# Kernel optimization log

Measured on AMD Instinct MI355X. Metric: run time of the kernel, lower is better.

Reference implementation:

```python
import jax, jax.numpy as jnp
import numpy as np

B, L, D, H, M = 4, 2048, 256, 8, 256
HEAD = D // H
EPS = 1e-6


def _pos_embedding(maxlen, d):
    i = np.arange(maxlen, dtype=np.float64)[:, None]
    j = np.arange(d, dtype=np.float64)[None, :]
    angle = i / np.power(10000.0, (j - (j % 2)) / d)
    pe = np.where(j % 2 == 0, np.sin(angle), np.cos(angle))
    return jnp.asarray(pe, jnp.float32)  # [L, D]


def _projection_matrix(m, d, seed=0):
    # FAVOR+ orthogonal random features: one full QR block (m == d here),
    # rows rescaled by norms of iid Gaussian rows (scaling=0 in source).
    rng = np.random.default_rng(seed)
    block = rng.standard_normal((d, d))
    q, _ = np.linalg.qr(block)
    q = q.T[:m]
    mult = np.linalg.norm(rng.standard_normal((m, d)), axis=1)
    return jnp.asarray(mult[:, None] * q, jnp.float32)  # [M, D]


def _softmax_kernel(x, is_query, proj):
    # x: [B, L, H, D], proj: [M, D]
    d = x.shape[-1]
    m = proj.shape[0]
    x = x * (float(d) ** -0.25)
    xp = jnp.einsum('blhd,md->blhm', x, proj)
    diag = 0.5 * jnp.sum(x * x, axis=-1, keepdims=True)
    if is_query:
        mx = jnp.max(xp, axis=-1, keepdims=True)
    else:
        mx = jnp.max(xp, axis=(-3, -1), keepdims=True)  # over L and M
    return (float(m) ** -0.5) * (jnp.exp(xp - diag - mx) + EPS)


def setup_inputs() -> dict:
    key = jax.random.key(0)
    ks = jax.random.split(key, 12)
    s = 1.0 / np.sqrt(D)
    inp = {
        'query': jax.random.normal(ks[0], (B, L, D), jnp.float32),
        'key': jax.random.normal(ks[1], (B, L, D), jnp.float32),
        'value': jax.random.normal(ks[2], (B, L, D), jnp.float32),
        'mask': jnp.ones((B, L), jnp.float32),
        'Wq': jax.random.normal(ks[3], (D, D), jnp.float32) * s,
        'bq': jnp.zeros((D,), jnp.float32),
        'Wk': jax.random.normal(ks[4], (D, D), jnp.float32) * s,
        'bk': jnp.zeros((D,), jnp.float32),
        'Wv': jax.random.normal(ks[5], (D, D), jnp.float32) * s,
        'bv': jnp.zeros((D,), jnp.float32),
        'Wo': jax.random.normal(ks[6], (D, D), jnp.float32) * s,
        'bo': jnp.zeros((D,), jnp.float32),
        'proj': _projection_matrix(M, D, seed=0),
        'pos': _pos_embedding(L, D),
    }
    return inp


def reference(query, key, value, mask, Wq, bq, Wk, bk, Wv, bv, Wo, bo, proj, pos):
    b = query.shape[0]
    q = query @ Wq + bq                      # [B, L, D]
    k = key @ Wk + bk
    v = value @ Wv + bv
    # per-head copies keep the FULL model_size feature dim (as in source)
    q = jnp.broadcast_to(q[:, :, None, :], (b, L, H, D))
    k = jnp.broadcast_to(k[:, :, None, :], (b, L, H, D))
    pos_b = pos[None]                        # [1, L, D]
    cos_pos = jnp.repeat(pos_b[..., None, 1::2], 2, axis=-1)  # [1, L, 1, D]
    sin_pos = jnp.repeat(pos_b[..., None, ::2], 2, axis=-1)

    def rot(x):
        x2 = jnp.stack([-x[..., 1::2], x[..., ::2]], axis=-1).reshape(x.shape)
        return x * cos_pos + x2 * sin_pos

    q = rot(q)
    k = rot(k)
    v = v.reshape(b, L, H, HEAD)

    qp = _softmax_kernel(q, True, proj)      # [B, L, H, M]
    kp = _softmax_kernel(k, False, proj)     # [B, L, H, M]

    kvs = jnp.einsum('blhm,blhd->bhmd', kp, v)
    num = jnp.einsum('blhm,bhmd->blhd', qp, kvs)
    den = jnp.einsum('blhm,bhm->blh', qp, jnp.sum(kp, axis=1))
    ctx = (num / den[..., None]).reshape(b, L, D)
    return ctx @ Wo + bo
```

## Files before the change

### kernel.cpp

```cpp
#include <hip/hip_runtime.h>

typedef unsigned short u16;
typedef unsigned int u32;
typedef __bf16 bf16x8 __attribute__((ext_vector_type(8)));
typedef float f32x4 __attribute__((ext_vector_type(4)));

__device__ __forceinline__ float bf2f(u16 u) { return __uint_as_float(((u32)u) << 16); }
__device__ __forceinline__ u16 f2bf(float f) {
  u32 x = __float_as_uint(f);
  x += 0x7fffu + ((x >> 16) & 1u);
  return (u16)(x >> 16);
}
__device__ __forceinline__ u32 encf(float x) {
  u32 u = __float_as_uint(x);
  return (u >> 31) ? ~u : (u | 0x80000000u);
}
__device__ __forceinline__ float decf(u32 e) {
  return (e >> 31) ? __uint_as_float(e & 0x7fffffffu) : __uint_as_float(~e);
}

#define MFMA(a, b, c) __builtin_amdgcn_mfma_f32_16x16x32_bf16(a, b, c, 0, 0, 0)

__global__ __launch_bounds__(256) void prep_w(
    const float* Wq, const float* Wk, const float* Wv, const float* Wo,
    const float* proj, const float* bv,
    u16* WqT, u16* WkT, u16* projb, u16* WWT, float* bw,
    float* __restrict__ ksum, u32* __restrict__ mxk) {
  __shared__ u16 tsh[32][33];
  __shared__ u16 As[64][40];
  __shared__ u16 Bs[64][40];
  const int z = blockIdx.z;
  const int x = threadIdx.x, y = threadIdx.y;
  const int tid = y * 32 + x;
  if (z < 2) {
    const float* s = z == 0 ? Wq : Wk;
    u16* d = z == 0 ? WqT : WkT;
    int r0 = blockIdx.y * 32, c0 = blockIdx.x * 32;
#pragma unroll
    for (int i = 0; i < 32; i += 8) tsh[y + i][x] = f2bf(s[(r0 + y + i) * 256 + c0 + x]);
    __syncthreads();
#pragma unroll
    for (int i = 0; i < 32; i += 8) d[(c0 + y + i) * 256 + r0 + x] = tsh[x][y + i];
    return;
  }
  if (z == 2) {
    int r0 = blockIdx.y * 32, c0 = blockIdx.x * 32;
#pragma unroll
    for (int i = 0; i < 32; i += 8)
      projb[(r0 + y + i) * 256 + c0 + x] = f2bf(proj[(r0 + y + i) * 256 + c0 + x]);
    return;
  }
  if (blockIdx.x < 4 && blockIdx.y < 4) {
    const int o0 = blockIdx.x * 64, i0 = blockIdx.y * 64;
    const int lane = tid & 63, wid = tid >> 6;
    const int wm = (wid >> 1) * 32, wn = (wid & 1) * 32;
    const int fm = lane & 15, fq = (lane >> 4) * 8, rowq = (lane >> 4) * 4;
    const int dr = tid >> 3, oc = (tid & 7) * 8;
    const int ir = tid >> 2, dc = (tid & 3) * 8;
    f32x4 acc[2][2] = {};
    for (int it = 0; it < 8; ++it) {
      int d0 = it * 32;
      float4 w0 = *(const float4*)(Wo + (d0 + dr) * 256 + o0 + oc);
      float4 w1 = *(const float4*)(Wo + (d0 + dr) * 256 + o0 + oc + 4);
      float4 v0 = *(const float4*)(Wv + (i0 + ir) * 256 + d0 + dc);
      float4 v1 = *(const float4*)(Wv + (i0 + ir) * 256 + d0 + dc + 4);
      __syncthreads();
      float wv[8] = {w0.x, w0.y, w0.z, w0.w, w1.x, w1.y, w1.z, w1.w};
#pragma unroll
      for (int j = 0; j < 8; ++j) As[oc + j][dr] = f2bf(wv[j]);
      u16* bp = &Bs[ir][dc];
      bp[0] = f2bf(v0.x); bp[1] = f2bf(v0.y); bp[2] = f2bf(v0.z); bp[3] = f2bf(v0.w);
      bp[4] = f2bf(v1.x); bp[5] = f2bf(v1.y); bp[6] = f2bf(v1.z); bp[7] = f2bf(v1.w);
      __syncthreads();
      bf16x8 a0 = *(const bf16x8*)&As[wm + fm][fq];
      bf16x8 a1 = *(const bf16x8*)&As[wm + 16 + fm][fq];
      bf16x8 b0 = *(const bf16x8*)&Bs[wn + fm][fq];
      bf16x8 b1 = *(const bf16x8*)&Bs[wn + 16 + fm][fq];
      acc[0][0] = MFMA(a0, b0, acc[0][0]);
      acc[0][1] = MFMA(a0, b1, acc[0][1]);
      acc[1][0] = MFMA(a1, b0, acc[1][0]);
      acc[1][1] = MFMA(a1, b1, acc[1][1]);
    }
#pragma unroll
    for (int mt = 0; mt < 2; ++mt)
#pragma unroll
      for (int nt = 0; nt < 2; ++nt)
#pragma unroll
        for (int r = 0; r < 4; ++r)
          WWT[(o0 + wm + mt * 16 + rowq + r) * 256 + i0 + wn + nt * 16 + fm] =
              f2bf(acc[mt][nt][r]);
    return;
  }
  if (blockIdx.x == 4 && blockIdx.y == 0) {
    float s = 0.0f;
    for (int d = 0; d < 256; ++d) s = fmaf(bv[d], Wo[d * 256 + tid], s);
    bw[tid] = s;
    for (int i = tid; i < 1024; i += 256) ksum[i] = 0.0f;
    if (tid < 4) mxk[tid] = 0u;
  }
}

__global__ __launch_bounds__(256, 3) void projrot2(
    const float* __restrict__ Xq, const float* __restrict__ Xk,
    const u16* __restrict__ WqT, const u16* __restrict__ WkT,
    const float* __restrict__ bq, const float* __restrict__ bk,
    const float* __restrict__ pos, const u16* __restrict__ projb,
    float* __restrict__ diag_k, u16* __restrict__ qp,
    float* __restrict__ xp, u32* __restrict__ mxk) {
  const int mode = blockIdx.z;
  const float* X = mode ? Xq : Xk;
  const u16* W = mode ? WqT : WkT;
  const float* bias = mode ? bq : bk;
  __shared__ u16 As[32][40];
  __shared__ u16 Bs[256][40];
  __shared__ u16 cbuf[32][264];
  __shared__ float dred[2][32];
  __shared__ float mred[2][32];
  __shared__ float wred[4];
  const int row0 = blockIdx.x * 32;
  const int t = threadIdx.x;
  const int lane = t & 63, wid = t >> 6;
  const int wrow = wid & 1, wcol = wid >> 1;
  const int fm = lane & 15, fq = (lane >> 4) * 8, rowq = (lane >> 4) * 4;
  const int ar = t >> 3, ak = (t & 7) * 4;

  f32x4 acc[8] = {};
  float4 av = *(const float4*)(X + (long long)(row0 + ar) * 256 + ak);
  uint4 bv0 = ((const uint4*)(W + (long long)t * 256))[0];
  uint4 bv1 = ((const uint4*)(W + (long long)t * 256))[1];
  uint4 bv2 = ((const uint4*)(W + (long long)t * 256))[2];
  uint4 bv3 = ((const uint4*)(W + (long long)t * 256))[3];
  for (int s = 0; s < 8; ++s) {
    __syncthreads();
    As[ar][ak] = f2bf(av.x); As[ar][ak + 1] = f2bf(av.y);
    As[ar][ak + 2] = f2bf(av.z); As[ar][ak + 3] = f2bf(av.w);
    uint4* bsp = (uint4*)&Bs[t][0];
    bsp[0] = bv0; bsp[1] = bv1; bsp[2] = bv2; bsp[3] = bv3;
    __syncthreads();
    if (s < 7) {
      const int k1 = (s + 1) * 32;
      av = *(const float4*)(X + (long long)(row0 + ar) * 256 + k1 + ak);
      const uint4* wn = (const uint4*)(W + (long long)t * 256 + k1);
      bv0 = wn[0]; bv1 = wn[1]; bv2 = wn[2]; bv3 = wn[3];
    }
    bf16x8 af = *(const bf16x8*)&As[wrow * 16 + fm][fq];
#pragma unroll
    for (int j = 0; j < 8; ++j) {
      bf16x8 bf = *(const bf16x8*)&Bs[wcol * 128 + j * 16 + fm][fq];
      acc[j] = MFMA(af, bf, acc[j]);
    }
  }

  float dsum[4] = {};
#pragma unroll
  for (int j = 0; j < 8; ++j) {
    float bb2 = bias[wcol * 128 + j * 16 + fm];
#pragma unroll
    for (int r = 0; r < 4; ++r) {
      float v = acc[j][r] + bb2;
      acc[j][r] = v;
      dsum[r] += v * v;
    }
  }
#pragma unroll
  for (int o = 1; o < 16; o <<= 1)
#pragma unroll
    for (int r = 0; r < 4; ++r) dsum[r] += __shfl_xor(dsum[r], o, 64);
  if (fm == 0) {
#pragma unroll
    for (int r = 0; r < 4; ++r) dred[wcol][wrow * 16 + rowq + r] = dsum[r];
  }
  __syncthreads();
  if (mode == 0 && t < 32) diag_k[row0 + t] = 0.03125f * (dred[0][t] + dred[1][t]);

#pragma unroll
  for (int j = 0; j < 8; ++j) {
    const int c = wcol * 128 + j * 16 + fm;
#pragma unroll
    for (int r = 0; r < 4; ++r) {
      const int row = wrow * 16 + rowq + r;
      const int l = (row0 + row) & 2047;
      float v = acc[j][r];
      float prt = __shfl_xor(v, 1, 64);
      float x2 = (fm & 1) ? prt : -prt;
      float2 cs = *(const float2*)(pos + (long long)l * 256 + (c & ~1));
      cbuf[row][c] = f2bf(0.25f * (v * cs.y + x2 * cs.x));
    }
  }

  f32x4 acc2[8] = {};
  uint4 pv0 = ((const uint4*)(projb + (long long)t * 256))[0];
  uint4 pv1 = ((const uint4*)(projb + (long long)t * 256))[1];
  uint4 pv2 = ((const uint4*)(projb + (long long)t * 256))[2];
  uint4 pv3 = ((const uint4*)(projb + (long long)t * 256))[3];
  for (int s = 0; s < 8; ++s) {
    __syncthreads();
    uint4* bsp = (uint4*)&Bs[t][0];
    bsp[0] = pv0; bsp[1] = pv1; bsp[2] = pv2; bsp[3] = pv3;
    __syncthreads();
    if (s < 7) {
      const uint4* pn = (const uint4*)(projb + (long long)t * 256 + (s + 1) * 32);
      pv0 = pn[0]; pv1 = pn[1]; pv2 = pn[2]; pv3 = pn[3];
    }
    bf16x8 af = *(const bf16x8*)&cbuf[wrow * 16 + fm][s * 32 + fq];
#pragma unroll
    for (int j = 0; j < 8; ++j) {
      bf16x8 bf = *(const bf16x8*)&Bs[wcol * 128 + j * 16 + fm][fq];
      acc2[j] = MFMA(af, bf, acc2[j]);
    }
  }

  if (mode == 1) {
    float m4[4] = {-3.0e38f, -3.0e38f, -3.0e38f, -3.0e38f};
#pragma unroll
    for (int j = 0; j < 8; ++j)
#pragma unroll
      for (int r = 0; r < 4; ++r) m4[r] = fmaxf(m4[r], acc2[j][r]);
#pragma unroll
    for (int o = 1; o < 16; o <<= 1)
#pragma unroll
      for (int r = 0; r < 4; ++r) m4[r] = fmaxf(m4[r], __shfl_xor(m4[r], o, 64));
    if (fm == 0) {
#pragma unroll
      for (int r = 0; r < 4; ++r) mred[wcol][wrow * 16 + rowq + r] = m4[r];
    }
    __syncthreads();
#pragma unroll
    for (int j = 0; j < 8; ++j) {
      const int col = wcol * 128 + j * 16 + fm;
#pragma unroll
      for (int r = 0; r < 4; ++r) {
        const int row = wrow * 16 + rowq + r;
        float mxr = fmaxf(mred[0][row], mred[1][row]);
        float dgr = 0.03125f * (dred[0][row] + dred[1][row]);
        float v = 0.0625f * (__expf(acc2[j][r] - dgr - mxr) + 1e-6f);
        qp[(long long)(row0 + row) * 256 + col] = f2bf(v);
      }
    }
  } else {
    float mx = -3.0e38f;
#pragma unroll
    for (int j = 0; j < 8; ++j) {
      int col = wcol * 128 + j * 16 + fm;
#pragma unroll
      for (int r = 0; r < 4; ++r) {
        float v = acc2[j][r];
        xp[(long long)(row0 + wrow * 16 + rowq + r) * 256 + col] = v;
        mx = fmaxf(mx, v);
      }
    }
#pragma unroll
    for (int o = 32; o > 0; o >>= 1) mx = fmaxf(mx, __shfl_xor(mx, o, 64));
    if (lane == 0) wred[wid] = mx;
    __syncthreads();
    if (t == 0) {
      float m = fmaxf(fmaxf(wred[0], wred[1]), fmaxf(wred[2], wred[3]));
      atomicMax(mxk + (row0 >> 11), encf(m));
    }
  }
}

__global__ __launch_bounds__(256) void kvs_raw_split(
    const float* __restrict__ xp, const float* __restrict__ Xv,
    const float* __restrict__ diag_k, const u32* __restrict__ mxk,
    float* __restrict__ part, float* __restrict__ ksum) {
  __shared__ union USM {
    struct { u16 As[64][40]; u16 Bs[64][40]; } s;
    float ksbuf[32][65];
  } sm;
  const int mxt = blockIdx.x, ny = blockIdx.y, z = blockIdx.z;
  const int b = z >> 2, kc = z & 3;
  const long long l0 = (long long)b * 2048 + kc * 512;
  const int t = threadIdx.x;
  const int lane = t & 63, wid = t >> 6;
  const int wrow = wid >> 1, wcol = wid & 1;
  const int fm = lane & 15, fq = (lane >> 4) * 8, rowq = (lane >> 4) * 4;
  const float mxv = decf(mxk[b]);
  const int sr = t >> 3, sc = (t & 7) * 8;
  f32x4 acc[2][2] = {};
  float ksp[8] = {};
  long long lrow = l0 + sr;
  float4 x0 = *(const float4*)(xp + lrow * 256 + mxt * 64 + sc);
  float4 x1 = *(const float4*)(xp + lrow * 256 + mxt * 64 + sc + 4);
  float4 v0 = *(const float4*)(Xv + lrow * 256 + ny * 64 + sc);
  float4 v1 = *(const float4*)(Xv + lrow * 256 + ny * 64 + sc + 4);
  float dgl = diag_k[lrow];
  for (int s = 0; s < 16; ++s) {
    float xv[8] = {x0.x, x0.y, x0.z, x0.w, x1.x, x1.y, x1.z, x1.w};
    float vv[8] = {v0.x, v0.y, v0.z, v0.w, v1.x, v1.y, v1.z, v1.w};
    u16 kpv[8], vpv[8];
#pragma unroll
    for (int j = 0; j < 8; ++j) {
      float v = 0.0625f * (__expf(xv[j] - dgl - mxv) + 1e-6f);
      kpv[j] = f2bf(v);
      ksp[j] += bf2f(kpv[j]);
      vpv[j] = f2bf(vv[j]);
    }
    __syncthreads();
#pragma unroll
    for (int j = 0; j < 8; ++j) {
      sm.s.As[sc + j][sr] = kpv[j];
      sm.s.Bs[sc + j][sr] = vpv[j];
    }
    __syncthreads();
    if (s < 15) {
      lrow = l0 + (s + 1) * 32 + sr;
      x0 = *(const float4*)(xp + lrow * 256 + mxt * 64 + sc);
      x1 = *(const float4*)(xp + lrow * 256 + mxt * 64 + sc + 4);
      v0 = *(const float4*)(Xv + lrow * 256 + ny * 64 + sc);
      v1 = *(const float4*)(Xv + lrow * 256 + ny * 64 + sc + 4);
      dgl = diag_k[lrow];
    }
    bf16x8 a0 = *(const bf16x8*)&sm.s.As[wrow * 32 + fm][fq];
    bf16x8 a1 = *(const bf16x8*)&sm.s.As[wrow * 32 + 16 + fm][fq];
    bf16x8 b0 = *(const bf16x8*)&sm.s.Bs[wcol * 32 + fm][fq];
    bf16x8 b1 = *(const bf16x8*)&sm.s.Bs[wcol * 32 + 16 + fm][fq];
    acc[0][0] = MFMA(a0, b0, acc[0][0]);
    acc[0][1] = MFMA(a0, b1, acc[0][1]);
    acc[1][0] = MFMA(a1, b0, acc[1][0]);
    acc[1][1] = MFMA(a1, b1, acc[1][1]);
  }
#pragma unroll
  for (int mt = 0; mt < 2; ++mt)
#pragma unroll
    for (int nt = 0; nt < 2; ++nt)
#pragma unroll
      for (int r = 0; r < 4; ++r)
        part[(long long)z * 65536 +
             (long long)(mxt * 64 + wrow * 32 + mt * 16 + rowq + r) * 256 +
             ny * 64 + wcol * 32 + nt * 16 + fm] = acc[mt][nt][r];
  __syncthreads();
#pragma unroll
  for (int j = 0; j < 8; ++j) sm.ksbuf[sr][sc + j] = ksp[j];
  __syncthreads();
  if (ny == 0 && t < 64) {
    float ssum = 0.0f;
    for (int r = 0; r < 32; ++r) ssum += sm.ksbuf[r][t];
    atomicAdd(ksum + b * 256 + mxt * 64 + t, ssum);
  }
}

__global__ __launch_bounds__(256) void kvsw(
    const u16* __restrict__ WWT, const float* __restrict__ part,
    const float* __restrict__ ksum, const float* __restrict__ bw,
    u16* __restrict__ kvsWT) {
  __shared__ u16 As[64][40];
  __shared__ u16 Bs[64][40];
  const int o0 = blockIdx.x * 64, m0 = blockIdx.y * 64, b = blockIdx.z;
  const int t = threadIdx.x;
  const int lane = t & 63, wid = t >> 6;
  const int wm = (wid >> 1) * 32, wn = (wid & 1) * 32;
  const int fm = lane & 15, fq = (lane >> 4) * 8, rowq = (lane >> 4) * 4;
  const int arow = t >> 2, acol = (t & 3) * 8;
  f32x4 acc[2][2] = {};
  for (int it = 0; it < 8; ++it) {
    int k0 = it * 32;
    uint4 av = *(const uint4*)(WWT + (o0 + arow) * 256 + k0 + acol);
    float4 s0 = {0, 0, 0, 0}, s1 = {0, 0, 0, 0};
#pragma unroll
    for (int kc = 0; kc < 4; ++kc) {
      const float* pp = part + (long long)(b * 4 + kc) * 65536 + (long long)(m0 + arow) * 256 + k0 + acol;
      float4 u0 = *(const float4*)(pp);
      float4 u1 = *(const float4*)(pp + 4);
      s0.x += u0.x; s0.y += u0.y; s0.z += u0.z; s0.w += u0.w;
      s1.x += u1.x; s1.y += u1.y; s1.z += u1.z; s1.w += u1.w;
    }
    __syncthreads();
    *(uint4*)&As[arow][acol] = av;
    u16* bp = &Bs[arow][acol];
    bp[0] = f2bf(s0.x); bp[1] = f2bf(s0.y); bp[2] = f2bf(s0.z); bp[3] = f2bf(s0.w);
    bp[4] = f2bf(s1.x); bp[5] = f2bf(s1.y); bp[6] = f2bf(s1.z); bp[7] = f2bf(s1.w);
    __syncthreads();
    bf16x8 a0 = *(const bf16x8*)&As[wm + fm][fq];
    bf16x8 a1 = *(const bf16x8*)&As[wm + 16 + fm][fq];
    bf16x8 b0 = *(const bf16x8*)&Bs[wn + fm][fq];
    bf16x8 b1 = *(const bf16x8*)&Bs[wn + 16 + fm][fq];
    acc[0][0] = MFMA(a0, b0, acc[0][0]);
    acc[0][1] = MFMA(a0, b1, acc[0][1]);
    acc[1][0] = MFMA(a1, b0, acc[1][0]);
    acc[1][1] = MFMA(a1, b1, acc[1][1]);
  }
#pragma unroll
  for (int mt = 0; mt < 2; ++mt)
#pragma unroll
    for (int nt = 0; nt < 2; ++nt) {
      int col = m0 + wn + nt * 16 + fm;
      float ksv = ksum[b * 256 + col];
#pragma unroll
      for (int r = 0; r < 4; ++r) {
        int row = o0 + wm + mt * 16 + rowq + r;
        float v = acc[mt][nt][r] + bw[row] * ksv;
        kvsWT[(long long)b * 65536 + (long long)row * 256 + col] = f2bf(v);
      }
    }
}

__global__ __launch_bounds__(256, 4) void numout(
    const u16* __restrict__ qp, const float* __restrict__ ksum,
    const u16* __restrict__ kvsWT, const float* __restrict__ bo,
    float* __restrict__ out) {
  __shared__ u16 As[16][40];
  __shared__ u16 Bs[256][40];
  __shared__ float ksm[256], dsh[16];
  const int row0 = blockIdx.x * 16;
  const int b = blockIdx.z;
  const long long qrow = (long long)b * 2048 + row0;
  const int t = threadIdx.x;
  const int lane = t & 63, wid = t >> 6;
  const int fm = lane & 15, fq = (lane >> 4) * 8, rowq = (lane >> 4) * 4;
  const int ar = t >> 4, ak = (t & 15) * 2;

  u32 a0 = *(const u32*)(qp + (qrow + ar) * 256 + ak);
  const u16* kvr = kvsWT + (long long)b * 65536 + (long long)t * 256;
  uint4 bv0 = ((const uint4*)kvr)[0];
  uint4 bv1 = ((const uint4*)kvr)[1];
  uint4 bv2 = ((const uint4*)kvr)[2];
  uint4 bv3 = ((const uint4*)kvr)[3];

  ksm[t] = ksum[b * 256 + t];
  const int prow = t >> 4, pc0 = (t & 15) * 16;
  const u16* qr = qp + (qrow + prow) * 256 + pc0;
  uint4 u0 = *(const uint4*)(qr);
  uint4 u1 = *(const uint4*)(qr + 8);
  __syncthreads();

  float denp = 0.0f;
  u32 uu[8] = {u0.x, u0.y, u0.z, u0.w, u1.x, u1.y, u1.z, u1.w};
#pragma unroll
  for (int j = 0; j < 8; ++j) {
    denp += bf2f((u16)(uu[j] & 0xffffu)) * ksm[pc0 + 2 * j];
    denp += bf2f((u16)(uu[j] >> 16)) * ksm[pc0 + 2 * j + 1];
  }
#pragma unroll
  for (int o = 1; o < 16; o <<= 1) denp += __shfl_xor(denp, o, 64);
  if ((t & 15) == 0) dsh[prow] = denp;

  f32x4 acc[4] = {};
  for (int s = 0; s < 8; ++s) {
    __syncthreads();
    *(u32*)&As[ar][ak] = a0;
    uint4* bsp = (uint4*)&Bs[t][0];
    bsp[0] = bv0; bsp[1] = bv1; bsp[2] = bv2; bsp[3] = bv3;
    __syncthreads();
    if (s < 7) {
      const int k1 = (s + 1) * 32;
      a0 = *(const u32*)(qp + (qrow + ar) * 256 + k1 + ak);
      const uint4* kn = (const uint4*)(kvr + k1);
      bv0 = kn[0]; bv1 = kn[1]; bv2 = kn[2]; bv3 = kn[3];
    }
    bf16x8 af = *(const bf16x8*)&As[fm][fq];
#pragma unroll
    for (int j = 0; j < 4; ++j) {
      bf16x8 bf = *(const bf16x8*)&Bs[wid * 64 + j * 16 + fm][fq];
      acc[j] = MFMA(af, bf, acc[j]);
    }
  }
#pragma unroll
  for (int j = 0; j < 4; ++j) {
    int col = wid * 64 + j * 16 + fm;
    float bb2 = bo[col];
#pragma unroll
    for (int r = 0; r < 4; ++r) {
      int l = rowq + r;
      out[(qrow + l) * 256 + col] = acc[j][r] / dsh[l] + bb2;
    }
  }
}

extern "C" void kernel_launch(void* const* d_in, const int* in_sizes, int n_in,
                              void* d_out, int out_size, void* d_ws, size_t ws_size,
                              hipStream_t stream) {
  (void)in_sizes; (void)n_in; (void)out_size; (void)ws_size;
  const float* query = (const float*)d_in[0];
  const float* key = (const float*)d_in[1];
  const float* value = (const float*)d_in[2];
  const float* Wq = (const float*)d_in[4];
  const float* bq = (const float*)d_in[5];
  const float* Wk = (const float*)d_in[6];
  const float* bk = (const float*)d_in[7];
  const float* Wv = (const float*)d_in[8];
  const float* bv = (const float*)d_in[9];
  const float* Wo = (const float*)d_in[10];
  const float* bo = (const float*)d_in[11];
  const float* proj = (const float*)d_in[12];
  const float* pos = (const float*)d_in[13];

  char* w = (char*)d_ws;
  u16* qp = (u16*)(w);
  float* xp = (float*)(w + (8 << 20));
  float* part = (float*)(w + (16 << 20));
  u16* kvsWT = (u16*)(w + (20 << 20));
  u16* WqT = (u16*)(w + (21 << 20));
  u16* WkT = WqT + 65536;
  u16* projb = WkT + 65536;
  u16* WWT = projb + 65536;
  float* diag_k = (float*)(w + (22 << 20));
  float* ksum = diag_k + 8192;
  float* bw = ksum + 1024;
  u32* mxk = (u32*)(bw + 256);

  prep_w<<<dim3(8, 8, 4), dim3(32, 8), 0, stream>>>(Wq, Wk, Wv, Wo, proj, bv,
                                                    WqT, WkT, projb, WWT, bw,
                                                    ksum, mxk);
  projrot2<<<dim3(256, 1, 2), dim3(256), 0, stream>>>(
      query, key, WqT, WkT, bq, bk, pos, projb, diag_k, qp, xp, mxk);
  kvs_raw_split<<<dim3(4, 4, 16), dim3(256), 0, stream>>>(xp, value, diag_k, mxk,
                                                          part, ksum);
  kvsw<<<dim3(4, 4, 4), dim3(256), 0, stream>>>(WWT, part, ksum, bw, kvsWT);
  numout<<<dim3(128, 1, 4), dim3(256), 0, stream>>>(qp, ksum, kvsWT, bo,
                                                    (float*)d_out);
}
```

Baseline: 81.12 us.

## Fuse all stages into one persistent kernel with grid-wide atomic barriers

Replaces the five separate kernel launches with a single 512-block persistent kernel. The stages (weight prep, Q/K projection with rotary and feature map, KV partial sums, KV times W reduction, output) are separated by software grid barriers built on an atomic counter. The k-split of the KV reduction also changes from 4 to 8 chunks per batch. This removes per-launch overhead and the inter-kernel gaps, but it relies on all 512 blocks being co-resident (launch bounds of 2 blocks per CU) and adds a memset plus spin-wait cost at each barrier.

New measurement: 250.9 us. +209.3%, slower.

```diff
diff --git a/kernel.cpp b/kernel.cpp
--- a/kernel.cpp
+++ b/kernel.cpp
@@ -21,61 +21,311 @@
 
 #define MFMA(a, b, c) __builtin_amdgcn_mfma_f32_16x16x32_bf16(a, b, c, 0, 0, 0)
 
-__global__ __launch_bounds__(256) void prep_w(
-    const float* Wq, const float* Wk, const float* Wv, const float* Wo,
-    const float* proj, const float* bv,
-    u16* WqT, u16* WkT, u16* projb, u16* WWT, float* bw,
-    float* __restrict__ ksum, u32* __restrict__ mxk) {
-  __shared__ u16 tsh[32][33];
-  __shared__ u16 As[64][40];
-  __shared__ u16 Bs[64][40];
-  const int z = blockIdx.z;
-  const int x = threadIdx.x, y = threadIdx.y;
-  const int tid = y * 32 + x;
-  if (z < 2) {
-    const float* s = z == 0 ? Wq : Wk;
-    u16* d = z == 0 ? WqT : WkT;
-    int r0 = blockIdx.y * 32, c0 = blockIdx.x * 32;
-#pragma unroll
-    for (int i = 0; i < 32; i += 8) tsh[y + i][x] = f2bf(s[(r0 + y + i) * 256 + c0 + x]);
+__device__ __forceinline__ void gbar(u32* cnt, u32 target) {
+  __syncthreads();
+  if (threadIdx.x == 0) {
+    __hip_atomic_fetch_add(cnt, 1u, __ATOMIC_RELEASE, __HIP_MEMORY_SCOPE_AGENT);
+    while (__hip_atomic_load(cnt, __ATOMIC_RELAXED, __HIP_MEMORY_SCOPE_AGENT) < target)
+      __builtin_amdgcn_s_sleep(2);
+    __threadfence();
+  }
+  __syncthreads();
+}
+
+struct MegaArgs {
+  const float* Xq; const float* Xk; const float* Xv;
+  const float* Wq; const float* bq; const float* Wk; const float* bk;
+  const float* Wv; const float* bv; const float* Wo; const float* bo;
+  const float* proj; const float* pos;
+  u16* WqT; u16* WkT; u16* projb; u16* WWT; u16* qp; u16* kvsWT;
+  float* xp; float* part; float* diag_k; float* ksum; float* bw;
+  u32* mxk; float* out; u32* bar;
+};
+
+union SMU {
+  struct { u16 tsh[32][33]; } t;
+  struct { u16 As[64][40]; u16 Bs[64][40]; } g;
+  struct { float ksbuf[32][65]; } k;
+  struct { u16 As[32][40]; u16 Bs[256][40]; u16 cbuf[32][264];
+           float dred[2][32]; float mred[2][32]; float wred[4]; } b;
+  struct { u16 As[64][40]; u16 Bs[16][40]; } d;
+  struct { u16 As[16][40]; u16 Bs[256][40];
+           float ksm[256]; float dsh[16]; } e;
+};
+
+__global__ __launch_bounds__(256, 2) void mega(MegaArgs a) {
+  __shared__ SMU sm;
+  const int bid = blockIdx.x;
+  const int t = threadIdx.x;
+
+  {
+    const int x = t & 31, y = t >> 5;
+    if (bid < 192) {
+      const int which = bid >> 6;
+      const int sub = bid & 63;
+      const int c0 = (sub & 7) * 32, r0 = (sub >> 3) * 32;
+      if (which < 2) {
+        const float* s = which == 0 ? a.Wq : a.Wk;
+        u16* d = which == 0 ? a.WqT : a.WkT;
+#pragma unroll
+        for (int i = 0; i < 32; i += 8)
+          sm.t.tsh[y + i][x] = f2bf(s[(r0 + y + i) * 256 + c0 + x]);
+        __syncthreads();
+#pragma unroll
+        for (int i = 0; i < 32; i += 8)
+          d[(c0 + y + i) * 256 + r0 + x] = sm.t.tsh[x][y + i];
+      } else {
+#pragma unroll
+        for (int i = 0; i < 32; i += 8)
+          a.projb[(r0 + y + i) * 256 + c0 + x] = f2bf(a.proj[(r0 + y + i) * 256 + c0 + x]);
+      }
+    } else if (bid < 208) {
+      const int sub = bid - 192;
+      const int o0 = (sub & 3) * 64, i0 = (sub >> 2) * 64;
+      const int lane = t & 63, wid = t >> 6;
+      const int wm = (wid >> 1) * 32, wn = (wid & 1) * 32;
+      const int fm = lane & 15, fq = (lane >> 4) * 8, rowq = (lane >> 4) * 4;
+      const int dr = t >> 3, oc = (t & 7) * 8;
+      const int ir = t >> 2, dc = (t & 3) * 8;
+      f32x4 acc[2][2] = {};
+      for (int it = 0; it < 8; ++it) {
+        int d0 = it * 32;
+        float4 w0 = *(const float4*)(a.Wo + (d0 + dr) * 256 + o0 + oc);
+        float4 w1 = *(const float4*)(a.Wo + (d0 + dr) * 256 + o0 + oc + 4);
+        float4 v0 = *(const float4*)(a.Wv + (i0 + ir) * 256 + d0 + dc);
+        float4 v1 = *(const float4*)(a.Wv + (i0 + ir) * 256 + d0 + dc + 4);
+        __syncthreads();
+        float wv[8] = {w0.x, w0.y, w0.z, w0.w, w1.x, w1.y, w1.z, w1.w};
+#pragma unroll
+        for (int j = 0; j < 8; ++j) sm.g.As[oc + j][dr] = f2bf(wv[j]);
+        u16* bp = &sm.g.Bs[ir][dc];
+        bp[0] = f2bf(v0.x); bp[1] = f2bf(v0.y); bp[2] = f2bf(v0.z); bp[3] = f2bf(v0.w);
+        bp[4] = f2bf(v1.x); bp[5] = f2bf(v1.y); bp[6] = f2bf(v1.z); bp[7] = f2bf(v1.w);
+        __syncthreads();
+        bf16x8 a0 = *(const bf16x8*)&sm.g.As[wm + fm][fq];
+        bf16x8 a1 = *(const bf16x8*)&sm.g.As[wm + 16 + fm][fq];
+        bf16x8 b0 = *(const bf16x8*)&sm.g.Bs[wn + fm][fq];
+        bf16x8 b1 = *(const bf16x8*)&sm.g.Bs[wn + 16 + fm][fq];
+        acc[0][0] = MFMA(a0, b0, acc[0][0]);
+        acc[0][1] = MFMA(a0, b1, acc[0][1]);
+        acc[1][0] = MFMA(a1, b0, acc[1][0]);
+        acc[1][1] = MFMA(a1, b1, acc[1][1]);
+      }
+#pragma unroll
+      for (int mt = 0; mt < 2; ++mt)
+#pragma unroll
+        for (int nt = 0; nt < 2; ++nt)
+#pragma unroll
+          for (int r = 0; r < 4; ++r)
+            a.WWT[(o0 + wm + mt * 16 + rowq + r) * 256 + i0 + wn + nt * 16 + fm] =
+                f2bf(acc[mt][nt][r]);
+    } else if (bid == 208) {
+      float s = 0.0f;
+      for (int d = 0; d < 256; ++d) s = fmaf(a.bv[d], a.Wo[d * 256 + t], s);
+      a.bw[t] = s;
+      for (int i = t; i < 1024; i += 256) a.ksum[i] = 0.0f;
+      if (t < 4) a.mxk[t] = 0u;
+    }
+  }
+  gbar(a.bar, 512);
+
+  {
+    const int mode = bid >> 8;
+    const int row0 = (bid & 255) * 32;
+    const float* X = mode ? a.Xq : a.Xk;
+    const u16* W = mode ? a.WqT : a.WkT;
+    const float* bias = mode ? a.bq : a.bk;
+    const int lane = t & 63, wid = t >> 6;
+    const int wrow = wid & 1, wcol = wid >> 1;
+    const int fm = lane & 15, fq = (lane >> 4) * 8, rowq = (lane >> 4) * 4;
+    const int ar = t >> 3, ak = (t & 7) * 4;
+
+    f32x4 acc[8] = {};
+    float4 av = *(const float4*)(X + (long long)(row0 + ar) * 256 + ak);
+    uint4 bv0 = ((const uint4*)(W + (long long)t * 256))[0];
+    uint4 bv1 = ((const uint4*)(W + (long long)t * 256))[1];
+    uint4 bv2 = ((const uint4*)(W + (long long)t * 256))[2];
+    uint4 bv3 = ((const uint4*)(W + (long long)t * 256))[3];
+    for (int s = 0; s < 8; ++s) {
+      __syncthreads();
+      sm.b.As[ar][ak] = f2bf(av.x); sm.b.As[ar][ak + 1] = f2bf(av.y);
+      sm.b.As[ar][ak + 2] = f2bf(av.z); sm.b.As[ar][ak + 3] = f2bf(av.w);
+      uint4* bsp = (uint4*)&sm.b.Bs[t][0];
+      bsp[0] = bv0; bsp[1] = bv1; bsp[2] = bv2; bsp[3] = bv3;
+      __syncthreads();
+      if (s < 7) {
+        const int k1 = (s + 1) * 32;
+        av = *(const float4*)(X + (long long)(row0 + ar) * 256 + k1 + ak);
+        const uint4* wn = (const uint4*)(W + (long long)t * 256 + k1);
+        bv0 = wn[0]; bv1 = wn[1]; bv2 = wn[2]; bv3 = wn[3];
+      }
+      bf16x8 af = *(const bf16x8*)&sm.b.As[wrow * 16 + fm][fq];
+#pragma unroll
+      for (int j = 0; j < 8; ++j) {
+        bf16x8 bf = *(const bf16x8*)&sm.b.Bs[wcol * 128 + j * 16 + fm][fq];
+        acc[j] = MFMA(af, bf, acc[j]);
+      }
+    }
+
+    float dsum[4] = {};
+#pragma unroll
+    for (int j = 0; j < 8; ++j) {
+      float bb2 = bias[wcol * 128 + j * 16 + fm];
+#pragma unroll
+      for (int r = 0; r < 4; ++r) {
+        float v = acc[j][r] + bb2;
+        acc[j][r] = v;
+        dsum[r] += v * v;
+      }
+    }
+#pragma unroll
+    for (int o = 1; o < 16; o <<= 1)
+#pragma unroll
+      for (int r = 0; r < 4; ++r) dsum[r] += __shfl_xor(dsum[r], o, 64);
+    if (fm == 0) {
+#pragma unroll
+      for (int r = 0; r < 4; ++r) sm.b.dred[wcol][wrow * 16 + rowq + r] = dsum[r];
+    }
     __syncthreads();
-#pragma unroll
-    for (int i = 0; i < 32; i += 8) d[(c0 + y + i) * 256 + r0 + x] = tsh[x][y + i];
-    return;
+    if (mode == 0 && t < 32)
+      a.diag_k[row0 + t] = 0.03125f * (sm.b.dred[0][t] + sm.b.dred[1][t]);
+
+#pragma unroll
+    for (int j = 0; j < 8; ++j) {
+      const int c = wcol * 128 + j * 16 + fm;
+#pragma unroll
+      for (int r = 0; r < 4; ++r) {
+        const int row = wrow * 16 + rowq + r;
+        const int l = (row0 + row) & 2047;
+        float v = acc[j][r];
+        float prt = __shfl_xor(v, 1, 64);
+        float x2 = (fm & 1) ? prt : -prt;
+        float2 cs = *(const float2*)(a.pos + (long long)l * 256 + (c & ~1));
+        sm.b.cbuf[row][c] = f2bf(0.25f * (v * cs.y + x2 * cs.x));
+      }
+    }
+
+    f32x4 acc2[8] = {};
+    uint4 pv0 = ((const uint4*)(a.projb + (long long)t * 256))[0];
+    uint4 pv1 = ((const uint4*)(a.projb + (long long)t * 256))[1];
+    uint4 pv2 = ((const uint4*)(a.projb + (long long)t * 256))[2];
+    uint4 pv3 = ((const uint4*)(a.projb + (long long)t * 256))[3];
+    for (int s = 0; s < 8; ++s) {
+      __syncthreads();
+      uint4* bsp = (uint4*)&sm.b.Bs[t][0];
+      bsp[0] = pv0; bsp[1] = pv1; bsp[2] = pv2; bsp[3] = pv3;
+      __syncthreads();
+      if (s < 7) {
+        const uint4* pn = (const uint4*)(a.projb + (long long)t * 256 + (s + 1) * 32);
+        pv0 = pn[0]; pv1 = pn[1]; pv2 = pn[2]; pv3 = pn[3];
+      }
+      bf16x8 af = *(const bf16x8*)&sm.b.cbuf[wrow * 16 + fm][s * 32 + fq];
+#pragma unroll
+      for (int j = 0; j < 8; ++j) {
+        bf16x8 bf = *(const bf16x8*)&sm.b.Bs[wcol * 128 + j * 16 + fm][fq];
+        acc2[j] = MFMA(af, bf, acc2[j]);
+      }
+    }
+
+    if (mode == 1) {
+      float m4[4] = {-3.0e38f, -3.0e38f, -3.0e38f, -3.0e38f};
+#pragma unroll
+      for (int j = 0; j < 8; ++j)
+#pragma unroll
+        for (int r = 0; r < 4; ++r) m4[r] = fmaxf(m4[r], acc2[j][r]);
+#pragma unroll
+      for (int o = 1; o < 16; o <<= 1)
+#pragma unroll
+        for (int r = 0; r < 4; ++r) m4[r] = fmaxf(m4[r], __shfl_xor(m4[r], o, 64));
+      if (fm == 0) {
+#pragma unroll
+        for (int r = 0; r < 4; ++r) sm.b.mred[wcol][wrow * 16 + rowq + r] = m4[r];
+      }
+      __syncthreads();
+#pragma unroll
+      for (int j = 0; j < 8; ++j) {
+        const int col = wcol * 128 + j * 16 + fm;
+#pragma unroll
+        for (int r = 0; r < 4; ++r) {
+          const int row = wrow * 16 + rowq + r;
+          float mxr = fmaxf(sm.b.mred[0][row], sm.b.mred[1][row]);
+          float dgr = 0.03125f * (sm.b.dred[0][row] + sm.b.dred[1][row]);
+          float v = 0.0625f * (__expf(acc2[j][r] - dgr - mxr) + 1e-6f);
+          a.qp[(long long)(row0 + row) * 256 + col] = f2bf(v);
+        }
+      }
+    } else {
+      float mx = -3.0e38f;
+#pragma unroll
+      for (int j = 0; j < 8; ++j) {
+        int col = wcol * 128 + j * 16 + fm;
+#pragma unroll
+        for (int r = 0; r < 4; ++r) {
+          float v = acc2[j][r];
+          a.xp[(long long)(row0 + wrow * 16 + rowq + r) * 256 + col] = v;
+          mx = fmaxf(mx, v);
+        }
+      }
+#pragma unroll
+      for (int o = 32; o > 0; o >>= 1) mx = fmaxf(mx, __shfl_xor(mx, o, 64));
+      if (lane == 0) sm.b.wred[wid] = mx;
+      __syncthreads();
+      if (t == 0) {
+        float m = fmaxf(fmaxf(sm.b.wred[0], sm.b.wred[1]),
+                        fmaxf(sm.b.wred[2], sm.b.wred[3]));
+        atomicMax(a.mxk + (row0 >> 11), encf(m));
+      }
+    }
   }
-  if (z == 2) {
-    int r0 = blockIdx.y * 32, c0 = blockIdx.x * 32;
-#pragma unroll
-    for (int i = 0; i < 32; i += 8)
-      projb[(r0 + y + i) * 256 + c0 + x] = f2bf(proj[(r0 + y + i) * 256 + c0 + x]);
-    return;
-  }
-  if (blockIdx.x < 4 && blockIdx.y < 4) {
-    const int o0 = blockIdx.x * 64, i0 = blockIdx.y * 64;
-    const int lane = tid & 63, wid = tid >> 6;
-    const int wm = (wid >> 1) * 32, wn = (wid & 1) * 32;
+  gbar(a.bar, 1024);
+
+  {
+    const int mxt = bid & 3, ny = (bid >> 2) & 3, z = bid >> 4;
+    const int b = z >> 3, kc = z & 7;
+    const long long l0 = (long long)b * 2048 + kc * 256;
+    const int lane = t & 63, wid = t >> 6;
+    const int wrow = wid >> 1, wcol = wid & 1;
     const int fm = lane & 15, fq = (lane >> 4) * 8, rowq = (lane >> 4) * 4;
-    const int dr = tid >> 3, oc = (tid & 7) * 8;
-    const int ir = tid >> 2, dc = (tid & 3) * 8;
+    const float mxv = decf(a.mxk[b]);
+    const int sr = t >> 3, sc = (t & 7) * 8;
     f32x4 acc[2][2] = {};
-    for (int it = 0; it < 8; ++it) {
-      int d0 = it * 32;
-      float4 w0 = *(const float4*)(Wo + (d0 + dr) * 256 + o0 + oc);
-      float4 w1 = *(const float4*)(Wo + (d0 + dr) * 256 + o0 + oc + 4);
-      float4 v0 = *(const float4*)(Wv + (i0 + ir) * 256 + d0 + dc);
-      float4 v1 = *(const float4*)(Wv + (i0 + ir) * 256 + d0 + dc + 4);
-      __syncthreads();
-      float wv[8] = {w0.x, w0.y, w0.z, w0.w, w1.x, w1.y, w1.z, w1.w};
-#pragma unroll
-      for (int j = 0; j < 8; ++j) As[oc + j][dr] = f2bf(wv[j]);
-      u16* bp = &Bs[ir][dc];
-      bp[0] = f2bf(v0.x); bp[1] = f2bf(v0.y); bp[2] = f2bf(v0.z); bp[3] = f2bf(v0.w);
-      bp[4] = f2bf(v1.x); bp[5] = f2bf(v1.y); bp[6] = f2bf(v1.z); bp[7] = f2bf(v1.w);
-      __syncthreads();
-      bf16x8 a0 = *(const bf16x8*)&As[wm + fm][fq];
-      bf16x8 a1 = *(const bf16x8*)&As[wm + 16 + fm][fq];
-      bf16x8 b0 = *(const bf16x8*)&Bs[wn + fm][fq];
-      bf16x8 b1 = *(const bf16x8*)&Bs[wn + 16 + fm][fq];
+    float ksp[8] = {};
+    long long lrow = l0 + sr;
+    float4 x0 = *(const float4*)(a.xp + lrow * 256 + mxt * 64 + sc);
+    float4 x1 = *(const float4*)(a.xp + lrow * 256 + mxt * 64 + sc + 4);
+    float4 v0 = *(const float4*)(a.Xv + lrow * 256 + ny * 64 + sc);
+    float4 v1 = *(const float4*)(a.Xv + lrow * 256 + ny * 64 + sc + 4);
+    float dgl = a.diag_k[lrow];
+    for (int s = 0; s < 8; ++s) {
+      float xv[8] = {x0.x, x0.y, x0.z, x0.w, x1.x, x1.y, x1.z, x1.w};
+      float vv[8] = {v0.x, v0.y, v0.z, v0.w, v1.x, v1.y, v1.z, v1.w};
+      u16 kpv[8], vpv[8];
+#pragma unroll
+      for (int j = 0; j < 8; ++j) {
+        float v = 0.0625f * (__expf(xv[j] - dgl - mxv) + 1e-6f);
+        kpv[j] = f2bf(v);
+        ksp[j] += bf2f(kpv[j]);
+        vpv[j] = f2bf(vv[j]);
+      }
+      __syncthreads();
+#pragma unroll
+      for (int j = 0; j < 8; ++j) {
+        sm.g.As[sc + j][sr] = kpv[j];
+        sm.g.Bs[sc + j][sr] = vpv[j];
+      }
+      __syncthreads();
+      if (s < 7) {
+        lrow = l0 + (s + 1) * 32 + sr;
+        x0 = *(const float4*)(a.xp + lrow * 256 + mxt * 64 + sc);
+        x1 = *(const float4*)(a.xp + lrow * 256 + mxt * 64 + sc + 4);
+        v0 = *(const float4*)(a.Xv + lrow * 256 + ny * 64 + sc);
+        v1 = *(const float4*)(a.Xv + lrow * 256 + ny * 64 + sc + 4);
+        dgl = a.diag_k[lrow];
+      }
+      bf16x8 a0 = *(const bf16x8*)&sm.g.As[wrow * 32 + fm][fq];
+      bf16x8 a1 = *(const bf16x8*)&sm.g.As[wrow * 32 + 16 + fm][fq];
+      bf16x8 b0 = *(const bf16x8*)&sm.g.Bs[wcol * 32 + fm][fq];
+      bf16x8 b1 = *(const bf16x8*)&sm.g.Bs[wcol * 32 + 16 + fm][fq];
       acc[0][0] = MFMA(a0, b0, acc[0][0]);
       acc[0][1] = MFMA(a0, b1, acc[0][1]);
       acc[1][0] = MFMA(a1, b0, acc[1][0]);
@@ -87,382 +337,130 @@
       for (int nt = 0; nt < 2; ++nt)
 #pragma unroll
         for (int r = 0; r < 4; ++r)
-          WWT[(o0 + wm + mt * 16 + rowq + r) * 256 + i0 + wn + nt * 16 + fm] =
-              f2bf(acc[mt][nt][r]);
-    return;
+          a.part[(long long)z * 65536 +
+                 (long long)(mxt * 64 + wrow * 32 + mt * 16 + rowq + r) * 256 +
+                 ny * 64 + wcol * 32 + nt * 16 + fm] = acc[mt][nt][r];
+    __syncthreads();
+#pragma unroll
+    for (int j = 0; j < 8; ++j) sm.k.ksbuf[sr][sc + j] = ksp[j];
+    __syncthreads();
+    if (ny == 0 && t < 64) {
+      float ssum = 0.0f;
+      for (int r = 0; r < 32; ++r) ssum += sm.k.ksbuf[r][t];
+      atomicAdd(a.ksum + b * 256 + mxt * 64 + t, ssum);
+    }
   }
-  if (blockIdx.x == 4 && blockIdx.y == 0) {
-    float s = 0.0f;
-    for (int d = 0; d < 256; ++d) s = fmaf(bv[d], Wo[d * 256 + tid], s);
-    bw[tid] = s;
-    for (int i = tid; i < 1024; i += 256) ksum[i] = 0.0f;
-    if (tid < 4) mxk[tid] = 0u;
+  gbar(a.bar, 1536);
+
+  if (bid < 256) {
+    const int b = bid >> 6;
+    const int o0 = ((bid >> 4) & 3) * 64;
+    const int m0 = (bid & 15) * 16;
+    const int w4 = t >> 6;
+    const int lane = t & 63;
+    const int fm = lane & 15, fq = (lane >> 4) * 8, rowq = (lane >> 4) * 4;
+    const int arow = t >> 2, acol = (t & 3) * 8;
+    const int brow = t >> 4, bcol = (t & 15) * 2;
+    f32x4 acc = {0.0f, 0.0f, 0.0f, 0.0f};
+    uint4 av = *(const uint4*)(a.WWT + (o0 + arow) * 256 + acol);
+    float2 ps[8];
+    {
+      const float* pb = a.part + (long long)(b * 8) * 65536 + (m0 + brow) * 256 + bcol;
+#pragma unroll
+      for (int kc = 0; kc < 8; ++kc) ps[kc] = *(const float2*)(pb + (long long)kc * 65536);
+    }
+    for (int s = 0; s < 8; ++s) {
+      float sx = ps[0].x + ps[1].x + ps[2].x + ps[3].x + ps[4].x + ps[5].x + ps[6].x + ps[7].x;
+      float sy = ps[0].y + ps[1].y + ps[2].y + ps[3].y + ps[4].y + ps[5].y + ps[6].y + ps[7].y;
+      __syncthreads();
+      *(uint4*)&sm.d.As[arow][acol] = av;
+      sm.d.Bs[brow][bcol] = f2bf(sx);
+      sm.d.Bs[brow][bcol + 1] = f2bf(sy);
+      __syncthreads();
+      if (s < 7) {
+        const int k1 = (s + 1) * 32;
+        av = *(const uint4*)(a.WWT + (o0 + arow) * 256 + k1 + acol);
+        const float* pb = a.part + (long long)(b * 8) * 65536 + (m0 + brow) * 256 + k1 + bcol;
+#pragma unroll
+        for (int kc = 0; kc < 8; ++kc) ps[kc] = *(const float2*)(pb + (long long)kc * 65536);
+      }
+      bf16x8 af = *(const bf16x8*)&sm.d.As[w4 * 16 + fm][fq];
+      bf16x8 bf = *(const bf16x8*)&sm.d.Bs[fm][fq];
+      acc = MFMA(af, bf, acc);
+    }
+    const int col = m0 + fm;
+    float ksv = a.ksum[b * 256 + col];
+#pragma unroll
+    for (int r = 0; r < 4; ++r) {
+      int row = o0 + w4 * 16 + rowq + r;
+      a.kvsWT[(long long)b * 65536 + (long long)row * 256 + col] =
+          f2bf(acc[r] + a.bw[row] * ksv);
+    }
   }
-}
-
-__global__ __launch_bounds__(256, 3) void projrot2(
-    const float* __restrict__ Xq, const float* __restrict__ Xk,
-    const u16* __restrict__ WqT, const u16* __restrict__ WkT,
-    const float* __restrict__ bq, const float* __restrict__ bk,
-    const float* __restrict__ pos, const u16* __restrict__ projb,
-    float* __restrict__ diag_k, u16* __restrict__ qp,
-    float* __restrict__ xp, u32* __restrict__ mxk) {
-  const int mode = blockIdx.z;
-  const float* X = mode ? Xq : Xk;
-  const u16* W = mode ? WqT : WkT;
-  const float* bias = mode ? bq : bk;
-  __shared__ u16 As[32][40];
-  __shared__ u16 Bs[256][40];
-  __shared__ u16 cbuf[32][264];
-  __shared__ float dred[2][32];
-  __shared__ float mred[2][32];
-  __shared__ float wred[4];
-  const int row0 = blockIdx.x * 32;
-  const int t = threadIdx.x;
-  const int lane = t & 63, wid = t >> 6;
-  const int wrow = wid & 1, wcol = wid >> 1;
-  const int fm = lane & 15, fq = (lane >> 4) * 8, rowq = (lane >> 4) * 4;
-  const int ar = t >> 3, ak = (t & 7) * 4;
-
-  f32x4 acc[8] = {};
-  float4 av = *(const float4*)(X + (long long)(row0 + ar) * 256 + ak);
-  uint4 bv0 = ((const uint4*)(W + (long long)t * 256))[0];
-  uint4 bv1 = ((const uint4*)(W + (long long)t * 256))[1];
-  uint4 bv2 = ((const uint4*)(W + (long long)t * 256))[2];
-  uint4 bv3 = ((const uint4*)(W + (long long)t * 256))[3];
-  for (int s = 0; s < 8; ++s) {
+  gbar(a.bar, 2048);
+
+  {
+    const int row0 = (bid & 127) * 16;
+    const int b = bid >> 7;
+    const long long qrow = (long long)b * 2048 + row0;
+    const int lane = t & 63, wid = t >> 6;
+    const int fm = lane & 15, fq = (lane >> 4) * 8, rowq = (lane >> 4) * 4;
+    const int ar = t >> 4, ak = (t & 15) * 2;
+
+    u32 a0 = *(const u32*)(a.qp + (qrow + ar) * 256 + ak);
+    const u16* kvr = a.kvsWT + (long long)b * 65536 + (long long)t * 256;
+    uint4 bv0 = ((const uint4*)kvr)[0];
+    uint4 bv1 = ((const uint4*)kvr)[1];
+    uint4 bv2 = ((const uint4*)kvr)[2];
+    uint4 bv3 = ((const uint4*)kvr)[3];
+
+    sm.e.ksm[t] = a.ksum[b * 256 + t];
+    const int prow = t >> 4, pc0 = (t & 15) * 16;
+    const u16* qr = a.qp + (qrow + prow) * 256 + pc0;
+    uint4 u0 = *(const uint4*)(qr);
+    uint4 u1 = *(const uint4*)(qr + 8);
     __syncthreads();
-    As[ar][ak] = f2bf(av.x); As[ar][ak + 1] = f2bf(av.y);
-    As[ar][ak + 2] = f2bf(av.z); As[ar][ak + 3] = f2bf(av.w);
-    uint4* bsp = (uint4*)&Bs[t][0];
-    bsp[0] = bv0; bsp[1] = bv1; bsp[2] = bv2; bsp[3] = bv3;
-    __syncthreads();
-    if (s < 7) {
-      const int k1 = (s + 1) * 32;
-      av = *(const float4*)(X + (long long)(row0 + ar) * 256 + k1 + ak);
-      const uint4* wn = (const uint4*)(W + (long long)t * 256 + k1);
-      bv0 = wn[0]; bv1 = wn[1]; bv2 = wn[2]; bv3 = wn[3];
-    }
-    bf16x8 af = *(const bf16x8*)&As[wrow * 16 + fm][fq];
+
+    float denp = 0.0f;
+    u32 uu[8] = {u0.x, u0.y, u0.z, u0.w, u1.x, u1.y, u1.z, u1.w};
 #pragma unroll
     for (int j = 0; j < 8; ++j) {
-      bf16x8 bf = *(const bf16x8*)&Bs[wcol * 128 + j * 16 + fm][fq];
-      acc[j] = MFMA(af, bf, acc[j]);
-    }
-  }
-
-  float dsum[4] = {};
-#pragma unroll
-  for (int j = 0; j < 8; ++j) {
-    float bb2 = bias[wcol * 128 + j * 16 + fm];
-#pragma unroll
-    for (int r = 0; r < 4; ++r) {
-      float v = acc[j][r] + bb2;
-      acc[j][r] = v;
-      dsum[r] += v * v;
-    }
-  }
-#pragma unroll
-  for (int o = 1; o < 16; o <<= 1)
-#pragma unroll
-    for (int r = 0; r < 4; ++r) dsum[r] += __shfl_xor(dsum[r], o, 64);
-  if (fm == 0) {
-#pragma unroll
-    for (int r = 0; r < 4; ++r) dred[wcol][wrow * 16 + rowq + r] = dsum[r];
-  }
-  __syncthreads();
-  if (mode == 0 && t < 32) diag_k[row0 + t] = 0.03125f * (dred[0][t] + dred[1][t]);
-
-#pragma unroll
-  for (int j = 0; j < 8; ++j) {
-    const int c = wcol * 128 + j * 16 + fm;
-#pragma unroll
-    for (int r = 0; r < 4; ++r) {
-      const int row = wrow * 16 + rowq + r;
-      const int l = (row0 + row) & 2047;
-      float v = acc[j][r];
-      float prt = __shfl_xor(v, 1, 64);
-      float x2 = (fm & 1) ? prt : -prt;
-      float2 cs = *(const float2*)(pos + (long long)l * 256 + (c & ~1));
-      cbuf[row][c] = f2bf(0.25f * (v * cs.y + x2 * cs.x));
-    }
-  }
-
-  f32x4 acc2[8] = {};
-  uint4 pv0 = ((const uint4*)(projb + (long long)t * 256))[0];
-  uint4 pv1 = ((const uint4*)(projb + (long long)t * 256))[1];
-  uint4 pv2 = ((const uint4*)(projb + (long long)t * 256))[2];
-  uint4 pv3 = ((const uint4*)(projb + (long long)t * 256))[3];
-  for (int s = 0; s < 8; ++s) {
-    __syncthreads();
-    uint4* bsp = (uint4*)&Bs[t][0];
-    bsp[0] = pv0; bsp[1] = pv1; bsp[2] = pv2; bsp[3] = pv3;
-    __syncthreads();
-    if (s < 7) {
-      const uint4* pn = (const uint4*)(projb + (long long)t * 256 + (s + 1) * 32);
-      pv0 = pn[0]; pv1 = pn[1]; pv2 = pn[2]; pv3 = pn[3];
-    }
-    bf16x8 af = *(const bf16x8*)&cbuf[wrow * 16 + fm][s * 32 + fq];
-#pragma unroll
-    for (int j = 0; j < 8; ++j) {
-      bf16x8 bf = *(const bf16x8*)&Bs[wcol * 128 + j * 16 + fm][fq];
-      acc2[j] = MFMA(af, bf, acc2[j]);
-    }
-  }
-
-  if (mode == 1) {
-    float m4[4] = {-3.0e38f, -3.0e38f, -3.0e38f, -3.0e38f};
-#pragma unroll
-    for (int j = 0; j < 8; ++j)
-#pragma unroll
-      for (int r = 0; r < 4; ++r) m4[r] = fmaxf(m4[r], acc2[j][r]);
-#pragma unroll
-    for (int o = 1; o < 16; o <<= 1)
-#pragma unroll
-      for (int r = 0; r < 4; ++r) m4[r] = fmaxf(m4[r], __shfl_xor(m4[r], o, 64));
-    if (fm == 0) {
-#pragma unroll
-      for (int r = 0; r < 4; ++r) mred[wcol][wrow * 16 + rowq + r] = m4[r];
-    }
-    __syncthreads();
-#pragma unroll
-    for (int j = 0; j < 8; ++j) {
-      const int col = wcol * 128 + j * 16 + fm;
+      denp += bf2f((u16)(uu[j] & 0xffffu)) * sm.e.ksm[pc0 + 2 * j];
+      denp += bf2f((u16)(uu[j] >> 16)) * sm.e.ksm[pc0 + 2 * j + 1];
+    }
+#pragma unroll
+    for (int o = 1; o < 16; o <<= 1) denp += __shfl_xor(denp, o, 64);
+    if ((t & 15) == 0) sm.e.dsh[prow] = denp;
+
+    f32x4 acc[4] = {};
+    for (int s = 0; s < 8; ++s) {
+      __syncthreads();
+      *(u32*)&sm.e.As[ar][ak] = a0;
+      uint4* bsp = (uint4*)&sm.e.Bs[t][0];
+      bsp[0] = bv0; bsp[1] = bv1; bsp[2] = bv2; bsp[3] = bv3;
+      __syncthreads();
+      if (s < 7) {
+        const int k1 = (s + 1) * 32;
+        a0 = *(const u32*)(a.qp + (qrow + ar) * 256 + k1 + ak);
+        const uint4* kn = (const uint4*)(kvr + k1);
+        bv0 = kn[0]; bv1 = kn[1]; bv2 = kn[2]; bv3 = kn[3];
+      }
+      bf16x8 af = *(const bf16x8*)&sm.e.As[fm][fq];
+#pragma unroll
+      for (int j = 0; j < 4; ++j) {
+        bf16x8 bf = *(const bf16x8*)&sm.e.Bs[wid * 64 + j * 16 + fm][fq];
+        acc[j] = MFMA(af, bf, acc[j]);
+      }
+    }
+#pragma unroll
+    for (int j = 0; j < 4; ++j) {
+      int col = wid * 64 + j * 16 + fm;
+      float bb2 = a.bo[col];
 #pragma unroll
       for (int r = 0; r < 4; ++r) {
-        const int row = wrow * 16 + rowq + r;
-        float mxr = fmaxf(mred[0][row], mred[1][row]);
-        float dgr = 0.03125f * (dred[0][row] + dred[1][row]);
-        float v = 0.0625f * (__expf(acc2[j][r] - dgr - mxr) + 1e-6f);
-        qp[(long long)(row0 + row) * 256 + col] = f2bf(v);
-      }
-    }
-  } else {
-    float mx = -3.0e38f;
-#pragma unroll
-    for (int j = 0; j < 8; ++j) {
-      int col = wcol * 128 + j * 16 + fm;
-#pragma unroll
-      for (int r = 0; r < 4; ++r) {
-        float v = acc2[j][r];
-        xp[(long long)(row0 + wrow * 16 + rowq + r) * 256 + col] = v;
-        mx = fmaxf(mx, v);
-      }
-    }
-#pragma unroll
-    for (int o = 32; o > 0; o >>= 1) mx = fmaxf(mx, __shfl_xor(mx, o, 64));
-    if (lane == 0) wred[wid] = mx;
-    __syncthreads();
-    if (t == 0) {
-      float m = fmaxf(fmaxf(wred[0], wred[1]), fmaxf(wred[2], wred[3]));
-      atomicMax(mxk + (row0 >> 11), encf(m));
-    }
-  }
-}
-
-__global__ __launch_bounds__(256) void kvs_raw_split(
-    const float* __restrict__ xp, const float* __restrict__ Xv,
-    const float* __restrict__ diag_k, const u32* __restrict__ mxk,
-    float* __restrict__ part, float* __restrict__ ksum) {
-  __shared__ union USM {
-    struct { u16 As[64][40]; u16 Bs[64][40]; } s;
-    float ksbuf[32][65];
-  } sm;
-  const int mxt = blockIdx.x, ny = blockIdx.y, z = blockIdx.z;
-  const int b = z >> 2, kc = z & 3;
-  const long long l0 = (long long)b * 2048 + kc * 512;
-  const int t = threadIdx.x;
-  const int lane = t & 63, wid = t >> 6;
-  const int wrow = wid >> 1, wcol = wid & 1;
-  const int fm = lane & 15, fq = (lane >> 4) * 8, rowq = (lane >> 4) * 4;
-  const float mxv = decf(mxk[b]);
-  const int sr = t >> 3, sc = (t & 7) * 8;
-  f32x4 acc[2][2] = {};
-  float ksp[8] = {};
-  long long lrow = l0 + sr;
-  float4 x0 = *(const float4*)(xp + lrow * 256 + mxt * 64 + sc);
-  float4 x1 = *(const float4*)(xp + lrow * 256 + mxt * 64 + sc + 4);
-  float4 v0 = *(const float4*)(Xv + lrow * 256 + ny * 64 + sc);
-  float4 v1 = *(const float4*)(Xv + lrow * 256 + ny * 64 + sc + 4);
-  float dgl = diag_k[lrow];
-  for (int s = 0; s < 16; ++s) {
-    float xv[8] = {x0.x, x0.y, x0.z, x0.w, x1.x, x1.y, x1.z, x1.w};
-    float vv[8] = {v0.x, v0.y, v0.z, v0.w, v1.x, v1.y, v1.z, v1.w};
-    u16 kpv[8], vpv[8];
-#pragma unroll
-    for (int j = 0; j < 8; ++j) {
-      float v = 0.0625f * (__expf(xv[j] - dgl - mxv) + 1e-6f);
-      kpv[j] = f2bf(v);
-      ksp[j] += bf2f(kpv[j]);
-      vpv[j] = f2bf(vv[j]);
-    }
-    __syncthreads();
-#pragma unroll
-    for (int j = 0; j < 8; ++j) {
-      sm.s.As[sc + j][sr] = kpv[j];
-      sm.s.Bs[sc + j][sr] = vpv[j];
-    }
-    __syncthreads();
-    if (s < 15) {
-      lrow = l0 + (s + 1) * 32 + sr;
-      x0 = *(const float4*)(xp + lrow * 256 + mxt * 64 + sc);
-      x1 = *(const float4*)(xp + lrow * 256 + mxt * 64 + sc + 4);
-      v0 = *(const float4*)(Xv + lrow * 256 + ny * 64 + sc);
-      v1 = *(const float4*)(Xv + lrow * 256 + ny * 64 + sc + 4);
-      dgl = diag_k[lrow];
-    }
-    bf16x8 a0 = *(const bf16x8*)&sm.s.As[wrow * 32 + fm][fq];
-    bf16x8 a1 = *(const bf16x8*)&sm.s.As[wrow * 32 + 16 + fm][fq];
-    bf16x8 b0 = *(const bf16x8*)&sm.s.Bs[wcol * 32 + fm][fq];
-    bf16x8 b1 = *(const bf16x8*)&sm.s.Bs[wcol * 32 + 16 + fm][fq];
-    acc[0][0] = MFMA(a0, b0, acc[0][0]);
-    acc[0][1] = MFMA(a0, b1, acc[0][1]);
-    acc[1][0] = MFMA(a1, b0, acc[1][0]);
-    acc[1][1] = MFMA(a1, b1, acc[1][1]);
-  }
-#pragma unroll
-  for (int mt = 0; mt < 2; ++mt)
-#pragma unroll
-    for (int nt = 0; nt < 2; ++nt)
-#pragma unroll
-      for (int r = 0; r < 4; ++r)
-        part[(long long)z * 65536 +
-             (long long)(mxt * 64 + wrow * 32 + mt * 16 + rowq + r) * 256 +
-             ny * 64 + wcol * 32 + nt * 16 + fm] = acc[mt][nt][r];
-  __syncthreads();
-#pragma unroll
-  for (int j = 0; j < 8; ++j) sm.ksbuf[sr][sc + j] = ksp[j];
-  __syncthreads();
-  if (ny == 0 && t < 64) {
-    float ssum = 0.0f;
-    for (int r = 0; r < 32; ++r) ssum += sm.ksbuf[r][t];
-    atomicAdd(ksum + b * 256 + mxt * 64 + t, ssum);
-  }
-}
-
-__global__ __launch_bounds__(256) void kvsw(
-    const u16* __restrict__ WWT, const float* __restrict__ part,
-    const float* __restrict__ ksum, const float* __restrict__ bw,
-    u16* __restrict__ kvsWT) {
-  __shared__ u16 As[64][40];
-  __shared__ u16 Bs[64][40];
-  const int o0 = blockIdx.x * 64, m0 = blockIdx.y * 64, b = blockIdx.z;
-  const int t = threadIdx.x;
-  const int lane = t & 63, wid = t >> 6;
-  const int wm = (wid >> 1) * 32, wn = (wid & 1) * 32;
-  const int fm = lane & 15, fq = (lane >> 4) * 8, rowq = (lane >> 4) * 4;
-  const int arow = t >> 2, acol = (t & 3) * 8;
-  f32x4 acc[2][2] = {};
-  for (int it = 0; it < 8; ++it) {
-    int k0 = it * 32;
-    uint4 av = *(const uint4*)(WWT + (o0 + arow) * 256 + k0 + acol);
-    float4 s0 = {0, 0, 0, 0}, s1 = {0, 0, 0, 0};
-#pragma unroll
-    for (int kc = 0; kc < 4; ++kc) {
-      const float* pp = part + (long long)(b * 4 + kc) * 65536 + (long long)(m0 + arow) * 256 + k0 + acol;
-      float4 u0 = *(const float4*)(pp);
-      float4 u1 = *(const float4*)(pp + 4);
-      s0.x += u0.x; s0.y += u0.y; s0.z += u0.z; s0.w += u0.w;
-      s1.x += u1.x; s1.y += u1.y; s1.z += u1.z; s1.w += u1.w;
-    }
-    __syncthreads();
-    *(uint4*)&As[arow][acol] = av;
-    u16* bp = &Bs[arow][acol];
-    bp[0] = f2bf(s0.x); bp[1] = f2bf(s0.y); bp[2] = f2bf(s0.z); bp[3] = f2bf(s0.w);
-    bp[4] = f2bf(s1.x); bp[5] = f2bf(s1.y); bp[6] = f2bf(s1.z); bp[7] = f2bf(s1.w);
-    __syncthreads();
-    bf16x8 a0 = *(const bf16x8*)&As[wm + fm][fq];
-    bf16x8 a1 = *(const bf16x8*)&As[wm + 16 + fm][fq];
-    bf16x8 b0 = *(const bf16x8*)&Bs[wn + fm][fq];
-    bf16x8 b1 = *(const bf16x8*)&Bs[wn + 16 + fm][fq];
-    acc[0][0] = MFMA(a0, b0, acc[0][0]);
-    acc[0][1] = MFMA(a0, b1, acc[0][1]);
-    acc[1][0] = MFMA(a1, b0, acc[1][0]);
-    acc[1][1] = MFMA(a1, b1, acc[1][1]);
-  }
-#pragma unroll
-  for (int mt = 0; mt < 2; ++mt)
-#pragma unroll
-    for (int nt = 0; nt < 2; ++nt) {
-      int col = m0 + wn + nt * 16 + fm;
-      float ksv = ksum[b * 256 + col];
-#pragma unroll
-      for (int r = 0; r < 4; ++r) {
-        int row = o0 + wm + mt * 16 + rowq + r;
-        float v = acc[mt][nt][r] + bw[row] * ksv;
-        kvsWT[(long long)b * 65536 + (long long)row * 256 + col] = f2bf(v);
-      }
-    }
-}
-
-__global__ __launch_bounds__(256, 4) void numout(
-    const u16* __restrict__ qp, const float* __restrict__ ksum,
-    const u16* __restrict__ kvsWT, const float* __restrict__ bo,
-    float* __restrict__ out) {
-  __shared__ u16 As[16][40];
-  __shared__ u16 Bs[256][40];
-  __shared__ float ksm[256], dsh[16];
-  const int row0 = blockIdx.x * 16;
-  const int b = blockIdx.z;
-  const long long qrow = (long long)b * 2048 + row0;
-  const int t = threadIdx.x;
-  const int lane = t & 63, wid = t >> 6;
-  const int fm = lane & 15, fq = (lane >> 4) * 8, rowq = (lane >> 4) * 4;
-  const int ar = t >> 4, ak = (t & 15) * 2;
-
-  u32 a0 = *(const u32*)(qp + (qrow + ar) * 256 + ak);
-  const u16* kvr = kvsWT + (long long)b * 65536 + (long long)t * 256;
-  uint4 bv0 = ((const uint4*)kvr)[0];
-  uint4 bv1 = ((const uint4*)kvr)[1];
-  uint4 bv2 = ((const uint4*)kvr)[2];
-  uint4 bv3 = ((const uint4*)kvr)[3];
-
-  ksm[t] = ksum[b * 256 + t];
-  const int prow = t >> 4, pc0 = (t & 15) * 16;
-  const u16* qr = qp + (qrow + prow) * 256 + pc0;
-  uint4 u0 = *(const uint4*)(qr);
-  uint4 u1 = *(const uint4*)(qr + 8);
-  __syncthreads();
-
-  float denp = 0.0f;
-  u32 uu[8] = {u0.x, u0.y, u0.z, u0.w, u1.x, u1.y, u1.z, u1.w};
-#pragma unroll
-  for (int j = 0; j < 8; ++j) {
-    denp += bf2f((u16)(uu[j] & 0xffffu)) * ksm[pc0 + 2 * j];
-    denp += bf2f((u16)(uu[j] >> 16)) * ksm[pc0 + 2 * j + 1];
-  }
-#pragma unroll
-  for (int o = 1; o < 16; o <<= 1) denp += __shfl_xor(denp, o, 64);
-  if ((t & 15) == 0) dsh[prow] = denp;
-
-  f32x4 acc[4] = {};
-  for (int s = 0; s < 8; ++s) {
-    __syncthreads();
-    *(u32*)&As[ar][ak] = a0;
-    uint4* bsp = (uint4*)&Bs[t][0];
-    bsp[0] = bv0; bsp[1] = bv1; bsp[2] = bv2; bsp[3] = bv3;
-    __syncthreads();
-    if (s < 7) {
-      const int k1 = (s + 1) * 32;
-      a0 = *(const u32*)(qp + (qrow + ar) * 256 + k1 + ak);
-      const uint4* kn = (const uint4*)(kvr + k1);
-      bv0 = kn[0]; bv1 = kn[1]; bv2 = kn[2]; bv3 = kn[3];
-    }
-    bf16x8 af = *(const bf16x8*)&As[fm][fq];
-#pragma unroll
-    for (int j = 0; j < 4; ++j) {
-      bf16x8 bf = *(const bf16x8*)&Bs[wid * 64 + j * 16 + fm][fq];
-      acc[j] = MFMA(af, bf, acc[j]);
-    }
-  }
-#pragma unroll
-  for (int j = 0; j < 4; ++j) {
-    int col = wid * 64 + j * 16 + fm;
-    float bb2 = bo[col];
-#pragma unroll
-    for (int r = 0; r < 4; ++r) {
-      int l = rowq + r;
-      out[(qrow + l) * 256 + col] = acc[j][r] / dsh[l] + bb2;
+        int l = rowq + r;
+        a.out[(qrow + l) * 256 + col] = acc[j][r] / sm.e.dsh[l] + bb2;
+      }
     }
   }
 }
@@ -471,42 +469,36 @@
                               void* d_out, int out_size, void* d_ws, size_t ws_size,
                               hipStream_t stream) {
   (void)in_sizes; (void)n_in; (void)out_size; (void)ws_size;
-  const float* query = (const float*)d_in[0];
-  const float* key = (const float*)d_in[1];
-  const float* value = (const float*)d_in[2];
-  const float* Wq = (const float*)d_in[4];
-  const float* bq = (const float*)d_in[5];
-  const float* Wk = (const float*)d_in[6];
-  const float* bk = (const float*)d_in[7];
-  const float* Wv = (const float*)d_in[8];
-  const float* bv = (const float*)d_in[9];
-  const float* Wo = (const float*)d_in[10];
-  const float* bo = (const float*)d_in[11];
-  const float* proj = (const float*)d_in[12];
-  const float* pos = (const float*)d_in[13];
-
   char* w = (char*)d_ws;
-  u16* qp = (u16*)(w);
-  float* xp = (float*)(w + (8 << 20));
-  float* part = (float*)(w + (16 << 20));
-  u16* kvsWT = (u16*)(w + (20 << 20));
-  u16* WqT = (u16*)(w + (21 << 20));
-  u16* WkT = WqT + 65536;
-  u16* projb = WkT + 65536;
-  u16* WWT = projb + 65536;
-  float* diag_k = (float*)(w + (22 << 20));
-  float* ksum = diag_k + 8192;
-  float* bw = ksum + 1024;
-  u32* mxk = (u32*)(bw + 256);
-
-  prep_w<<<dim3(8, 8, 4), dim3(32, 8), 0, stream>>>(Wq, Wk, Wv, Wo, proj, bv,
-                                                    WqT, WkT, projb, WWT, bw,
-                                                    ksum, mxk);
-  projrot2<<<dim3(256, 1, 2), dim3(256), 0, stream>>>(
-      query, key, WqT, WkT, bq, bk, pos, projb, diag_k, qp, xp, mxk);
-  kvs_raw_split<<<dim3(4, 4, 16), dim3(256), 0, stream>>>(xp, value, diag_k, mxk,
-                                                          part, ksum);
-  kvsw<<<dim3(4, 4, 4), dim3(256), 0, stream>>>(WWT, part, ksum, bw, kvsWT);
-  numout<<<dim3(128, 1, 4), dim3(256), 0, stream>>>(qp, ksum, kvsWT, bo,
-                                                    (float*)d_out);
+  MegaArgs ma;
+  ma.Xq = (const float*)d_in[0];
+  ma.Xk = (const float*)d_in[1];
+  ma.Xv = (const float*)d_in[2];
+  ma.Wq = (const float*)d_in[4];
+  ma.bq = (const float*)d_in[5];
+  ma.Wk = (const float*)d_in[6];
+  ma.bk = (const float*)d_in[7];
+  ma.Wv = (const float*)d_in[8];
+  ma.bv = (const float*)d_in[9];
+  ma.Wo = (const float*)d_in[10];
+  ma.bo = (const float*)d_in[11];
+  ma.proj = (const float*)d_in[12];
+  ma.pos = (const float*)d_in[13];
+  ma.qp = (u16*)(w);
+  ma.xp = (float*)(w + (4 << 20));
+  ma.part = (float*)(w + (12 << 20));
+  ma.kvsWT = (u16*)(w + (20 << 20));
+  ma.WqT = (u16*)(w + (21 << 20));
+  ma.WkT = ma.WqT + 65536;
+  ma.projb = ma.WkT + 65536;
+  ma.WWT = ma.projb + 65536;
+  ma.diag_k = (float*)(w + (22 << 20));
+  ma.ksum = ma.diag_k + 8192;
+  ma.bw = ma.ksum + 1024;
+  ma.mxk = (u32*)(ma.bw + 256);
+  ma.bar = (u32*)(w + (23 << 20));
+  ma.out = (float*)d_out;
+
+  hipMemsetAsync(ma.bar, 0, 64, stream);
+  mega<<<dim3(512), dim3(256), 0, stream>>>(ma);
 }
```
